# Kernel tuning notes

Hardware: AMD Instinct MI355X
Metric: run time of the kernel (lower is better)

The kernel has to match this reference:

```python
import jax, jax.numpy as jnp
import numpy as np

B, L, D = 4, 1024, 1024
H, DK, DV = 16, 64, 64
TEMP = float(np.power(DK, 0.5))
LN_EPS = 1e-5


def setup_inputs() -> dict:
    key = jax.random.key(0)
    ks = jax.random.split(key, 11)
    s_qk = np.sqrt(2.0 / (D + DK))
    s_v = np.sqrt(2.0 / (D + DV))
    inp = {
        'q_in': jax.random.normal(ks[0], (B, L, D), jnp.float32),
        'k_in': jax.random.normal(ks[1], (B, L, D), jnp.float32),
        'v_in': jax.random.normal(ks[2], (B, L, D), jnp.float32),
        'Wq':  jax.random.normal(ks[3], (D, H * DK), jnp.float32) * s_qk,
        'Wq2': jax.random.normal(ks[4], (D, H * DK), jnp.float32) * s_qk,
        'Wk':  jax.random.normal(ks[5], (D, H * DK), jnp.float32) * s_qk,
        'Wv':  jax.random.normal(ks[6], (D, H * DV), jnp.float32) * s_v,
        'Wo':  jax.random.normal(ks[7], (H * DV, D), jnp.float32) * np.sqrt(2.0 / (H * DV + D)),
        'ln_g': jnp.ones((D,), jnp.float32),
        'ln_b': jnp.zeros((D,), jnp.float32),
        'Er':  jax.random.normal(ks[8], (H, L, DK), jnp.float32),
        # causal mask: True above the diagonal (positions to be masked with -inf)
        'mask': jnp.triu(jnp.ones((L, L), jnp.bool_), k=1)[None].repeat(B, axis=0),
    }
    return inp


def _skew(rel):
    # rel: [H, B, Lq, Lr] with Lr == Lq. Music-Transformer skew:
    # pad one zero column on the left, reshape, drop first row.
    h, b, lq, lr = rel.shape
    rel = jnp.pad(rel, ((0, 0), (0, 0), (0, 0), (1, 0)))        # [H,B,Lq,Lr+1]
    rel = rel.reshape(h, b, lr + 1, lq)                          # [H,B,Lr+1,Lq]
    return rel[:, :, 1:, :].reshape(h, b, lq, lr)                # [H,B,Lq,Lr]


def reference(q_in, k_in, v_in, Wq, Wq2, Wk, Wv, Wo, ln_g, ln_b, Er, mask):
    residual = q_in
    # projections -> [H, B, L, d]
    def proj(x, W, d):
        return x.reshape(B * L, D).dot(W).reshape(B, L, H, d).transpose(2, 0, 1, 3)
    q = proj(q_in, Wq, DK)
    q2 = proj(q_in, Wq2, DK)
    k = proj(k_in, Wk, DK)
    v = proj(v_in, Wv, DV)

    attn = jnp.einsum('hbqd,hbkd->hbqk', q, k) / TEMP            # [H,B,Lq,Lk]
    rel = _skew(jnp.einsum('hbqd,hrd->hbqr', q2, Er)) / TEMP     # [H,B,Lq,Lk]

    m = mask[None]                                               # [1,B,Lq,Lk]
    neg = jnp.float32(-jnp.inf)
    attn = jnp.where(m, neg, attn)
    rel = jnp.where(m, neg, rel)
    p = jax.nn.softmax(attn + rel, axis=-1)                      # [H,B,Lq,Lk]

    out = jnp.einsum('hbqk,hbkd->hbqd', p, v)                    # [H,B,Lq,DV]
    out = out.transpose(1, 2, 0, 3).reshape(B, L, H * DV)
    out = out.dot(Wo)                                            # dropout is identity (eval)

    x = out + residual
    mu = x.mean(-1, keepdims=True)
    var = x.var(-1, keepdims=True)
    y = (x - mu) * jax.lax.rsqrt(var + LN_EPS) * ln_g + ln_b
    return y, p
```

## Files before the change

kernel.cpp:

```cpp
#include <hip/hip_runtime.h>

typedef __bf16 bf16;
typedef __bf16 v8bf __attribute__((ext_vector_type(8)));
typedef float v4f __attribute__((ext_vector_type(4)));
typedef unsigned int v4u __attribute__((ext_vector_type(4)));

#define B_ 4
#define L_ 1024
#define D_ 1024
#define NEG (-3.0e38f)
#define MFMA16(a, b, c) __builtin_amdgcn_mfma_f32_16x16x32_bf16(a, b, c, 0, 0, 0)

#define SWZ(base, r, cb) ((char*)(base) + ((r) * 128) + ((cb) ^ (((r) & 7) << 4)))

typedef const __attribute__((address_space(1))) void* gas_t;
typedef __attribute__((address_space(3))) void* las_t;
__device__ __forceinline__ void gl_lds16(const bf16* g, bf16* l)
{
    __builtin_amdgcn_global_load_lds((gas_t)g, (las_t)l, 16, 0, 0);
}

__global__ __launch_bounds__(256) void wconv_kernel(
    const float* __restrict__ w0, const float* __restrict__ w1,
    const float* __restrict__ w2, const float* __restrict__ w3,
    const float* __restrict__ w4, const float* __restrict__ er,
    const float* __restrict__ qin, const float* __restrict__ kin,
    const float* __restrict__ vin,
    bf16* __restrict__ wt, bf16* __restrict__ erb,
    bf16* __restrict__ qbf, bf16* __restrict__ kbf, bf16* __restrict__ vbf)
{
    int z = blockIdx.z;
    int tx = threadIdx.x, ty = threadIdx.y;
    if (z < 5) {
        const float* src = z == 0 ? w0 : z == 1 ? w1 : z == 2 ? w2 : z == 3 ? w3 : w4;
        bf16* dst = wt + (size_t)z * 1024 * 1024;
        __shared__ float t[32][33];
        int bx = blockIdx.x * 32, by = blockIdx.y * 32;
#pragma unroll
        for (int i = 0; i < 4; i++)
            t[ty + i * 8][tx] = src[(size_t)(by + ty + i * 8) * 1024 + bx + tx];
        __syncthreads();
#pragma unroll
        for (int i = 0; i < 4; i++)
            dst[(size_t)(bx + ty + i * 8) * 1024 + by + tx] = (bf16)t[tx][ty + i * 8];
    } else if (z == 5) {
        int base = (blockIdx.y * 32 + blockIdx.x) * 256 + ty * 32 + tx;
#pragma unroll
        for (int i = 0; i < 4; i++) {
            int idx = base + i * 262144;
            erb[idx] = (bf16)er[idx];
        }
    } else {
        const float* src = z == 6 ? qin : z == 7 ? kin : vin;
        bf16* dst = z == 6 ? qbf : z == 7 ? kbf : vbf;
        int id = (blockIdx.y * 32 + blockIdx.x) * 256 + ty * 32 + tx;
#pragma unroll
        for (int i = 0; i < 4; i++) {
            int j = id * 4 + i * 1048576;
            float4 v = *(const float4*)(src + j);
            union { bf16 h[4]; uint2 u; } t;
            t.h[0] = (bf16)v.x; t.h[1] = (bf16)v.y;
            t.h[2] = (bf16)v.z; t.h[3] = (bf16)v.w;
            *(uint2*)(dst + j) = t.u;
        }
    }
}

__device__ __forceinline__ void gemm128_core(
    const bf16* __restrict__ Ab, const bf16* __restrict__ Bt,
    float* __restrict__ Cf, bf16* __restrict__ Cb, bf16* __restrict__ Cb2,
    int K, int mode, int tn, int tm,
    bf16* __restrict__ As , bf16* __restrict__ Bs )
{
    int tid = threadIdx.x, lane = tid & 63, w = tid >> 6;
    int wm = (w & 1) * 64, wn = (w >> 1) * 64;
    int m15 = lane & 15, rq = lane >> 4, kq = rq * 8;

    v4f acc[4][4];
#pragma unroll
    for (int m = 0; m < 4; ++m)
#pragma unroll
        for (int n = 0; n < 4; ++n)
#pragma unroll
            for (int i = 0; i < 4; ++i) acc[m][n][i] = 0.f;

    int sr = lane >> 2, scb = (lane & 3) * 8;
    const bf16* ga = Ab + (size_t)(tm + w * 32 + sr) * K + scb;
    const bf16* gb = Bt + (size_t)(tn + w * 32 + sr) * K + scb;
    bf16* la = As + w * 32 * 32;
    bf16* lb = Bs + w * 32 * 32;
    const size_t rowskip = (size_t)16 * K;

    for (int k0 = 0; k0 < K; k0 += 32) {
        gl_lds16(ga + k0, la);
        gl_lds16(ga + k0 + rowskip, la + 512);
        gl_lds16(gb + k0, lb);
        gl_lds16(gb + k0 + rowskip, lb + 512);
        __syncthreads();

        v8bf a[4], bfr[4];
#pragma unroll
        for (int m = 0; m < 4; ++m)
            a[m] = *(const v8bf*)&As[(wm + m * 16 + m15) * 32 + kq];
#pragma unroll
        for (int n = 0; n < 4; ++n)
            bfr[n] = *(const v8bf*)&Bs[(wn + n * 16 + m15) * 32 + kq];
#pragma unroll
        for (int m = 0; m < 4; ++m)
#pragma unroll
            for (int n = 0; n < 4; ++n)
                acc[m][n] = MFMA16(a[m], bfr[n], acc[m][n]);
        __syncthreads();
    }

#pragma unroll
    for (int m = 0; m < 4; ++m)
#pragma unroll
        for (int n = 0; n < 4; ++n) {
            int col = tn + wn + n * 16 + m15;
            if (mode == 2) {
                union { bf16 h[4]; uint2 u; } pk;
#pragma unroll
                for (int i = 0; i < 4; ++i) pk.h[i] = (bf16)acc[m][n][i];
                int row0 = tm + wm + m * 16 + rq * 4;
                int bb2 = row0 >> 10, l = row0 & 1023, hh = col >> 6, dv = col & 63;
                *(uint2*)&Cb[(((size_t)(bb2 * 16 + hh) * 64 + dv) << 10) + l] = pk.u;
            } else {
#pragma unroll
                for (int i = 0; i < 4; ++i) {
                    int row = tm + wm + m * 16 + rq * 4 + i;
                    float v = acc[m][n][i];
                    if (mode == 1) Cf[(size_t)row * 1024 + col] = v;
                    else {
                        bf16* dst = col < 1024 ? Cb : Cb2;
                        dst[(size_t)row * 1024 + (col & 1023)] = (bf16)v;
                    }
                }
            }
        }
}

__global__ __launch_bounds__(256) void gemm_proj(
    const bf16* __restrict__ qbf, const bf16* __restrict__ kbf,
    const bf16* __restrict__ vbf, const bf16* __restrict__ wT,
    bf16* __restrict__ qb, bf16* __restrict__ q2b,
    bf16* __restrict__ kb, bf16* __restrict__ vtb)
{
    __shared__ __align__(16) bf16 As[128 * 32];
    __shared__ __align__(16) bf16 Bs[128 * 32];
    int bx = blockIdx.x, tm = blockIdx.y * 128;
    const size_t MB = 1024 * 1024;
    if (bx < 16)
        gemm128_core(qbf, wT, nullptr, qb, q2b, 1024, 0, bx * 128, tm, As, Bs);
    else if (bx < 24)
        gemm128_core(kbf, wT + 2 * MB, nullptr, kb, nullptr, 1024, 0,
                     (bx - 16) * 128, tm, As, Bs);
    else
        gemm128_core(vbf, wT + 3 * MB, nullptr, vtb, nullptr, 1024, 2,
                     (bx - 24) * 128, tm, As, Bs);
}

__global__ __launch_bounds__(256) void gemm_out(
    const bf16* __restrict__ ab, const bf16* __restrict__ woT,
    float* __restrict__ y0)
{
    __shared__ __align__(16) bf16 As[128 * 32];
    __shared__ __align__(16) bf16 Bs[128 * 32];
    gemm128_core(ab, woT, y0, nullptr, nullptr, 1024, 1,
                 blockIdx.x * 128, blockIdx.y * 128, As, Bs);
}

__global__ __launch_bounds__(256, 2) void attn_mfma(
    const bf16* __restrict__ qb, const bf16* __restrict__ q2b,
    const bf16* __restrict__ kb, const bf16* __restrict__ vt,
    const bf16* __restrict__ erb, float* __restrict__ p_out,
    bf16* __restrict__ ab)
{
    int lin = blockIdx.x;
    int bh  = (lin & 7) | ((lin >> 6) << 3);
    int pp  = (lin >> 3) & 7;
    int h = bh >> 2, b = bh & 3;
    int tid = threadIdx.x, lane = tid & 63, w = tid >> 6;
    int m15 = lane & 15, rq = lane >> 4, kq = rq * 8;
    int li0 = w * 16 + rq * 4;

    __shared__ __align__(16) char KsB[2][8192];
    __shared__ __align__(16) char VtsB[2][8192];
    __shared__ __align__(16) char ErsB[3][8192];
    __shared__ __align__(16) float RELs[64][68];
    char* RELsB = (char*)RELs;

    size_t pb = (size_t)(h * 4 + b) << 20;
    size_t kbase = ((size_t)(b << 10) * 16 + h) * 64;
    size_t vbase = ((size_t)(b * 16 + h) << 16);
    const bf16* erh = erb + ((size_t)h << 16);

    int c0 = tid, c1 = tid + 256;
    int r0s = c0 >> 3, col0 = (c0 & 7) * 8, cb0 = (c0 & 7) * 16;
    int r1s = c1 >> 3, col1 = (c1 & 7) * 8, cb1 = (c1 & 7) * 16;

#define LOADK(d0, d1, kt) { int kk = (kt) << 6; \
    d0 = *(const uint4*)&kb[kbase + ((size_t)(kk + r0s) << 10) + col0]; \
    d1 = *(const uint4*)&kb[kbase + ((size_t)(kk + r1s) << 10) + col1]; }
#define LOADE(d0, d1, t) { const bf16* e = erh + ((size_t)(t) << 12); \
    d0 = *(const uint4*)&e[(r0s << 6) + col0]; \
    d1 = *(const uint4*)&e[(r1s << 6) + col1]; }
#define LOADV(d0, d1, kt) { int kk = (kt) << 6; \
    d0 = *(const uint4*)&vt[vbase + ((size_t)r0s << 10) + kk + col0]; \
    d1 = *(const uint4*)&vt[vbase + ((size_t)r1s << 10) + kk + col1]; }
#define STORE2(buf, v0, v1) { *(uint4*)SWZ(buf, r0s, cb0) = v0; \
                              *(uint4*)SWZ(buf, r1s, cb1) = v1; }

    for (int qs = 0; qs < 2; ++qs) {
        int qt = qs ? pp : 15 - pp;
        int q0 = qt << 6, nkt = qt + 1, t0 = 15 - qt;

        {
            int zr = tid >> 2, zc = (tid & 3) * 16;
            v4f zz = {0.f, 0.f, 0.f, 0.f};
            for (int kt = qt + 1; kt < 16; ++kt) {
                float* basep = p_out + pb + ((size_t)(q0 + zr) << 10) + kt * 64 + zc;
#pragma unroll
                for (int i = 0; i < 4; ++i)
                    __builtin_nontemporal_store(zz, (v4f*)(basep + i * 4));
            }
        }

        {
            uint4 a0 = *(const uint4*)&qb[((size_t)((b << 10) + q0 + r0s) * 16 + h) * 64 + col0];
            uint4 a1 = *(const uint4*)&qb[((size_t)((b << 10) + q0 + r1s) * 16 + h) * 64 + col1];
            uint4 b0 = *(const uint4*)&q2b[((size_t)((b << 10) + q0 + r0s) * 16 + h) * 64 + col0];
            uint4 b1 = *(const uint4*)&q2b[((size_t)((b << 10) + q0 + r1s) * 16 + h) * 64 + col1];
            STORE2(RELsB, a0, a1);
            STORE2(RELsB + 8192, b0, b1);
        }
        __syncthreads();
        v8bf alo  = *(const v8bf*)SWZ(RELsB,        w * 16 + m15, kq * 2);
        v8bf ahi  = *(const v8bf*)SWZ(RELsB,        w * 16 + m15, kq * 2 + 64);
        v8bf a2lo = *(const v8bf*)SWZ(RELsB + 8192, w * 16 + m15, kq * 2);
        v8bf a2hi = *(const v8bf*)SWZ(RELsB + 8192, w * 16 + m15, kq * 2 + 64);

        float m_run[4], l_run[4], linv[4];
#pragma unroll
        for (int i = 0; i < 4; ++i) { m_run[i] = NEG; l_run[i] = 0.f; }
        v4f oacc[4];
#pragma unroll
        for (int t = 0; t < 4; ++t)
#pragma unroll
            for (int i = 0; i < 4; ++i) oacc[t][i] = 0.f;

        for (int pass = 0; pass < 2; ++pass) {
            if (pass) {
#pragma unroll
                for (int i = 0; i < 4; ++i) linv[i] = 1.f / l_run[i];
            }
            {
                uint4 ka, kb2, e0a, e0b, e1a, e1b, va, vb2;
                LOADK(ka, kb2, 0);
                LOADE(e0a, e0b, t0);
                bool hb = (t0 + 1) <= 15;
                if (hb) LOADE(e1a, e1b, t0 + 1);
                if (pass) LOADV(va, vb2, 0);
                STORE2(KsB[0], ka, kb2);
                STORE2(ErsB[t0 % 3], e0a, e0b);
                if (hb) STORE2(ErsB[(t0 + 1) % 3], e1a, e1b);
                if (pass) STORE2(VtsB[0], va, vb2);
            }
            __syncthreads();

            uint4 nk0, nk1, ne0, ne1, nv0, nv1;
            for (int kt = 0; kt < nkt; ++kt) {
                int k0 = kt << 6;
                int tA = t0 + kt;
                bool hasB = tA < 15;
                bool hasNext = (kt + 1) < nkt;
                bool hasNE = hasNext && (tA + 2) <= 15;
                if (hasNext) {
                    LOADK(nk0, nk1, kt + 1);
                    if (hasNE) LOADE(ne0, ne1, tA + 2);
                    if (pass) LOADV(nv0, nv1, kt + 1);
                }
                char* Kb = KsB[kt & 1];
                char* EA = ErsB[tA % 3];
                char* EB = ErsB[(tA + 1) % 3];
                char* Vb = VtsB[kt & 1];

                __builtin_amdgcn_s_setprio(1);
#pragma unroll
                for (int ct = 0; ct < 4; ++ct) {
                    v4f a4 = {0.f, 0.f, 0.f, 0.f};
                    v8bf blo = *(const v8bf*)SWZ(EA, ct * 16 + m15, kq * 2);
                    v8bf bhi = *(const v8bf*)SWZ(EA, ct * 16 + m15, kq * 2 + 64);
                    a4 = MFMA16(a2lo, blo, a4);
                    a4 = MFMA16(a2hi, bhi, a4);
                    int c = ct * 16 + m15;
#pragma unroll
                    for (int i = 0; i < 4; ++i) {
                        int kl = c + li0 + i - 63;
                        if (kl >= 0) RELs[li0 + i][kl] = a4[i];
                    }
                }
                if (hasB) {
#pragma unroll
                    for (int ct = 0; ct < 4; ++ct) {
                        v4f a4 = {0.f, 0.f, 0.f, 0.f};
                        v8bf blo = *(const v8bf*)SWZ(EB, ct * 16 + m15, kq * 2);
                        v8bf bhi = *(const v8bf*)SWZ(EB, ct * 16 + m15, kq * 2 + 64);
                        a4 = MFMA16(a2lo, blo, a4);
                        a4 = MFMA16(a2hi, bhi, a4);
                        int c = ct * 16 + m15;
#pragma unroll
                        for (int i = 0; i < 4; ++i) {
                            int kl = c + li0 + i + 1;
                            if (kl < 64) RELs[li0 + i][kl] = a4[i];
                        }
                    }
                }
                v4f qk[4];
#pragma unroll
                for (int ct = 0; ct < 4; ++ct) {
                    v4f a4 = {0.f, 0.f, 0.f, 0.f};
                    v8bf blo = *(const v8bf*)SWZ(Kb, ct * 16 + m15, kq * 2);
                    v8bf bhi = *(const v8bf*)SWZ(Kb, ct * 16 + m15, kq * 2 + 64);
                    a4 = MFMA16(alo, blo, a4);
                    qk[ct] = MFMA16(ahi, bhi, a4);
                }
                __builtin_amdgcn_s_setprio(0);

                float sc[4][4];
#pragma unroll
                for (int ct = 0; ct < 4; ++ct)
#pragma unroll
                    for (int i = 0; i < 4; ++i) {
                        int li = li0 + i;
                        int j = ct * 16 + m15;
                        float v = (qk[ct][i] + RELs[li][j]) * 0.125f;
                        if (!hasB) v = (j > li) ? NEG : v;
                        sc[ct][i] = v;
                    }
                if (!pass) {
#pragma unroll
                    for (int i = 0; i < 4; ++i) {
                        float tmax = fmaxf(fmaxf(sc[0][i], sc[1][i]), fmaxf(sc[2][i], sc[3][i]));
#pragma unroll
                        for (int off = 1; off < 16; off <<= 1)
                            tmax = fmaxf(tmax, __shfl_xor(tmax, off));
                        float mn = fmaxf(m_run[i], tmax);
                        float es = __expf(sc[0][i] - mn) + __expf(sc[1][i] - mn)
                                 + __expf(sc[2][i] - mn) + __expf(sc[3][i] - mn);
#pragma unroll
                        for (int off = 1; off < 16; off <<= 1)
                            es += __shfl_xor(es, off);
                        l_run[i] = l_run[i] * __expf(m_run[i] - mn) + es;
                        m_run[i] = mn;
                    }
                } else {
#pragma unroll
                    for (int ct = 0; ct < 4; ++ct)
#pragma unroll
                        for (int i = 0; i < 4; ++i) {
                            int li = li0 + i;
                            int j = ct * 16 + m15;
                            RELs[li][j] = __expf(sc[ct][i] - m_run[i]) * linv[i];
                        }
                    asm volatile("" ::: "memory");
#pragma unroll
                    for (int i2 = 0; i2 < 2; ++i2)
#pragma unroll
                        for (int jh = 0; jh < 2; ++jh) {
                            int rr = w * 16 + (lane >> 3) + 8 * i2;
                            v4u val = *(const v4u*)(RELsB + rr * 272 + (lane & 7) * 16 + 128 * jh);
                            __builtin_nontemporal_store(val,
                                (v4u*)(p_out + pb + ((size_t)(q0 + rr) << 10) + k0 + (lane & 7) * 4 + 32 * jh));
                        }
                    const float* pr = &RELs[w * 16 + m15][0];
                    v4f f0 = *(const v4f*)(pr + kq);
                    v4f f1 = *(const v4f*)(pr + kq + 4);
                    v4f f2 = *(const v4f*)(pr + kq + 32);
                    v4f f3 = *(const v4f*)(pr + kq + 36);
                    v8bf plo, phi;
#pragma unroll
                    for (int j = 0; j < 4; ++j) {
                        plo[j] = (bf16)f0[j]; plo[j + 4] = (bf16)f1[j];
                        phi[j] = (bf16)f2[j]; phi[j + 4] = (bf16)f3[j];
                    }
                    __builtin_amdgcn_s_setprio(1);
#pragma unroll
                    for (int ct = 0; ct < 4; ++ct) {
                        v8bf blo = *(const v8bf*)SWZ(Vb, ct * 16 + m15, kq * 2);
                        v8bf bhi = *(const v8bf*)SWZ(Vb, ct * 16 + m15, kq * 2 + 64);
                        oacc[ct] = MFMA16(plo, blo, oacc[ct]);
                        oacc[ct] = MFMA16(phi, bhi, oacc[ct]);
                    }
                    __builtin_amdgcn_s_setprio(0);
                }
                if (hasNext) {
                    STORE2(KsB[(kt + 1) & 1], nk0, nk1);
                    if (hasNE) STORE2(ErsB[(tA + 2) % 3], ne0, ne1);
                    if (pass) STORE2(VtsB[(kt + 1) & 1], nv0, nv1);
                }
                __syncthreads();
            }
        }

#pragma unroll
        for (int ct = 0; ct < 4; ++ct)
#pragma unroll
            for (int i = 0; i < 4; ++i)
                ab[((size_t)((b << 10) + q0 + li0 + i) * 16 + h) * 64 + ct * 16 + m15] =
                    (bf16)oacc[ct][i];
    }
#undef LOADK
#undef LOADE
#undef LOADV
#undef STORE2
}

__global__ __launch_bounds__(256) void ln_kernel(
    const float* __restrict__ y0, const float* __restrict__ res,
    const float* __restrict__ g, const float* __restrict__ bb,
    float* __restrict__ y)
{
    int row = blockIdx.x, tid = threadIdx.x, lane = tid & 63, w = tid >> 6;
    __shared__ float rs[4], rq2[4];
    const float* xr = y0 + (size_t)row * D_;
    const float* rr = res + (size_t)row * D_;
    float x[4], sum = 0.f, sq = 0.f;
#pragma unroll
    for (int i = 0; i < 4; i++) {
        int c = tid + i * 256;
        x[i] = xr[c] + rr[c];
        sum += x[i]; sq += x[i] * x[i];
    }
#pragma unroll
    for (int off = 32; off; off >>= 1) { sum += __shfl_xor(sum, off); sq += __shfl_xor(sq, off); }
    if (lane == 0) { rs[w] = sum; rq2[w] = sq; }
    __syncthreads();
    sum = rs[0] + rs[1] + rs[2] + rs[3];
    sq  = rq2[0] + rq2[1] + rq2[2] + rq2[3];
    float mean = sum * (1.f / D_);
    float var  = sq * (1.f / D_) - mean * mean;
    float inv  = rsqrtf(var + 1e-5f);
#pragma unroll
    for (int i = 0; i < 4; i++) {
        int c = tid + i * 256;
        y[(size_t)row * D_ + c] = (x[i] - mean) * inv * g[c] + bb[c];
    }
}

extern "C" void kernel_launch(void* const* d_in, const int* in_sizes, int n_in,
                              void* d_out, int out_size, void* d_ws, size_t ws_size,
                              hipStream_t stream)
{
    const float* q_in = (const float*)d_in[0];
    const float* k_in = (const float*)d_in[1];
    const float* v_in = (const float*)d_in[2];
    const float* Wq   = (const float*)d_in[3];
    const float* Wq2  = (const float*)d_in[4];
    const float* Wk   = (const float*)d_in[5];
    const float* Wv   = (const float*)d_in[6];
    const float* Wo   = (const float*)d_in[7];
    const float* ln_g = (const float*)d_in[8];
    const float* ln_b = (const float*)d_in[9];
    const float* Er   = (const float*)d_in[10];

    float* y_out = (float*)d_out;
    float* p_out = y_out + (size_t)B_ * L_ * D_;

    char* ws = (char*)d_ws;
    const size_t MB = 1024 * 1024;
    bf16*  wT  = (bf16*)(ws);
    bf16*  erb = (bf16*)(ws + 10 * MB);
    bf16*  qb  = (bf16*)(ws + 12 * MB);
    bf16*  q2b = (bf16*)(ws + 20 * MB);
    bf16*  kb  = (bf16*)(ws + 28 * MB);
    bf16*  vtb = (bf16*)(ws + 36 * MB);
    bf16*  ab  = (bf16*)(ws + 44 * MB);
    float* y0  = (float*)(ws + 52 * MB);

    bf16* qbf = (bf16*)((char*)p_out + 160 * MB);
    bf16* kbf = (bf16*)((char*)p_out + 168 * MB);
    bf16* vbf = (bf16*)((char*)p_out + 176 * MB);

    wconv_kernel<<<dim3(32, 32, 9), dim3(32, 8), 0, stream>>>(
        Wq, Wq2, Wk, Wv, Wo, Er, q_in, k_in, v_in, wT, erb, qbf, kbf, vbf);

    gemm_proj<<<dim3(32, 32), 256, 0, stream>>>(qbf, kbf, vbf, wT,
                                                qb, q2b, kb, vtb);

    attn_mfma<<<dim3(512), dim3(256), 0, stream>>>(qb, q2b, kb, vtb, erb, p_out, ab);

    gemm_out<<<dim3(8, 32), 256, 0, stream>>>(ab, wT + 4 * MB, y0);
    ln_kernel<<<4096, 256, 0, stream>>>(y0, q_in, ln_g, ln_b, y_out);
}
```

Measured before the change: 606.7 us.

## Split attention into one block per q-tile, load Er from global, retile output GEMM

The attention kernel now launches one block per (head, batch, q-tile), 1024 blocks, instead of pairing a long and a short q-tile per block. It raises the occupancy hint to 3 blocks per CU and drops the Er LDS triple buffer, so Er fragments are read straight from global memory into MFMA operands. The output projection gets its own 64x128 tiled GEMM, double-buffered via global_load_lds, with twice as many blocks. The aim is more parallelism and occupancy and less LDS. The cost is uncoalesced, uncached-in-LDS Er reads and a heavier tail from the largest q-tiles, which no longer share a block with short ones.

```diff
diff --git a/kernel.cpp b/kernel.cpp
--- a/kernel.cpp
+++ b/kernel.cpp
@@ -161,32 +161,87 @@
 }
 
 __global__ __launch_bounds__(256) void gemm_out(
-    const bf16* __restrict__ ab, const bf16* __restrict__ woT,
-    float* __restrict__ y0)
-{
-    __shared__ __align__(16) bf16 As[128 * 32];
-    __shared__ __align__(16) bf16 Bs[128 * 32];
-    gemm128_core(ab, woT, y0, nullptr, nullptr, 1024, 1,
-                 blockIdx.x * 128, blockIdx.y * 128, As, Bs);
-}
-
-__global__ __launch_bounds__(256, 2) void attn_mfma(
+    const bf16* __restrict__ Ab, const bf16* __restrict__ Bt,
+    float* __restrict__ Cf)
+{
+    const int K = 1024;
+    __shared__ __align__(16) bf16 As[2][64 * 32];
+    __shared__ __align__(16) bf16 Bs[2][128 * 32];
+    int tid = threadIdx.x, lane = tid & 63, w = tid >> 6;
+    int tn = blockIdx.x * 128, tm = blockIdx.y * 64;
+    int wn = w * 32;
+    int m15 = lane & 15, rq = lane >> 4, kq = rq * 8;
+
+    v4f acc[4][2];
+#pragma unroll
+    for (int m = 0; m < 4; ++m)
+#pragma unroll
+        for (int n = 0; n < 2; ++n)
+#pragma unroll
+            for (int i = 0; i < 4; ++i) acc[m][n][i] = 0.f;
+
+    int sr = lane >> 2, sc8 = (lane & 3) * 8;
+    const bf16* ga  = Ab + (size_t)(tm + w * 16 + sr) * K + sc8;
+    const bf16* gb0 = Bt + (size_t)(tn + w * 32 + sr) * K + sc8;
+    const bf16* gb1 = gb0 + (size_t)16 * K;
+
+#define GSTAGE(buf, k0s) { \
+    gl_lds16(ga  + (k0s), As[buf] + w * 16 * 32); \
+    gl_lds16(gb0 + (k0s), Bs[buf] + w * 32 * 32); \
+    gl_lds16(gb1 + (k0s), Bs[buf] + (w * 32 + 16) * 32); }
+
+    int cur = 0;
+    GSTAGE(0, 0);
+    __syncthreads();
+    for (int k0 = 0; k0 < K; k0 += 32) {
+        if (k0 + 32 < K) GSTAGE(cur ^ 1, k0 + 32);
+        v8bf a[4], bb[2];
+#pragma unroll
+        for (int m = 0; m < 4; ++m)
+            a[m] = *(const v8bf*)&As[cur][(m * 16 + m15) * 32 + kq];
+#pragma unroll
+        for (int n = 0; n < 2; ++n)
+            bb[n] = *(const v8bf*)&Bs[cur][(wn + n * 16 + m15) * 32 + kq];
+#pragma unroll
+        for (int m = 0; m < 4; ++m)
+#pragma unroll
+            for (int n = 0; n < 2; ++n)
+                acc[m][n] = MFMA16(a[m], bb[n], acc[m][n]);
+        __syncthreads();
+        cur ^= 1;
+    }
+#undef GSTAGE
+
+#pragma unroll
+    for (int m = 0; m < 4; ++m)
+#pragma unroll
+        for (int n = 0; n < 2; ++n) {
+            int col = tn + wn + n * 16 + m15;
+#pragma unroll
+            for (int i = 0; i < 4; ++i) {
+                int row = tm + m * 16 + rq * 4 + i;
+                Cf[(size_t)row * 1024 + col] = acc[m][n][i];
+            }
+        }
+}
+
+__global__ __launch_bounds__(256, 3) void attn_mfma(
     const bf16* __restrict__ qb, const bf16* __restrict__ q2b,
     const bf16* __restrict__ kb, const bf16* __restrict__ vt,
     const bf16* __restrict__ erb, float* __restrict__ p_out,
     bf16* __restrict__ ab)
 {
     int lin = blockIdx.x;
-    int bh  = (lin & 7) | ((lin >> 6) << 3);
-    int pp  = (lin >> 3) & 7;
+    int bh  = lin & 63;
+    int qt  = 15 - (lin >> 6);
     int h = bh >> 2, b = bh & 3;
+    int q0 = qt << 6, nkt = qt + 1, t0 = 15 - qt;
     int tid = threadIdx.x, lane = tid & 63, w = tid >> 6;
     int m15 = lane & 15, rq = lane >> 4, kq = rq * 8;
     int li0 = w * 16 + rq * 4;
 
     __shared__ __align__(16) char KsB[2][8192];
     __shared__ __align__(16) char VtsB[2][8192];
-    __shared__ __align__(16) char ErsB[3][8192];
     __shared__ __align__(16) float RELs[64][68];
     char* RELsB = (char*)RELs;
 
@@ -202,216 +257,197 @@
 #define LOADK(d0, d1, kt) { int kk = (kt) << 6; \
     d0 = *(const uint4*)&kb[kbase + ((size_t)(kk + r0s) << 10) + col0]; \
     d1 = *(const uint4*)&kb[kbase + ((size_t)(kk + r1s) << 10) + col1]; }
-#define LOADE(d0, d1, t) { const bf16* e = erh + ((size_t)(t) << 12); \
-    d0 = *(const uint4*)&e[(r0s << 6) + col0]; \
-    d1 = *(const uint4*)&e[(r1s << 6) + col1]; }
 #define LOADV(d0, d1, kt) { int kk = (kt) << 6; \
     d0 = *(const uint4*)&vt[vbase + ((size_t)r0s << 10) + kk + col0]; \
     d1 = *(const uint4*)&vt[vbase + ((size_t)r1s << 10) + kk + col1]; }
 #define STORE2(buf, v0, v1) { *(uint4*)SWZ(buf, r0s, cb0) = v0; \
                               *(uint4*)SWZ(buf, r1s, cb1) = v1; }
 
-    for (int qs = 0; qs < 2; ++qs) {
-        int qt = qs ? pp : 15 - pp;
-        int q0 = qt << 6, nkt = qt + 1, t0 = 15 - qt;
-
+    {
+        int zr = tid >> 2, zc = (tid & 3) * 16;
+        v4f zz = {0.f, 0.f, 0.f, 0.f};
+        for (int kt = qt + 1; kt < 16; ++kt) {
+            float* basep = p_out + pb + ((size_t)(q0 + zr) << 10) + kt * 64 + zc;
+#pragma unroll
+            for (int i = 0; i < 4; ++i)
+                __builtin_nontemporal_store(zz, (v4f*)(basep + i * 4));
+        }
+    }
+
+    {
+        uint4 a0 = *(const uint4*)&qb[((size_t)((b << 10) + q0 + r0s) * 16 + h) * 64 + col0];
+        uint4 a1 = *(const uint4*)&qb[((size_t)((b << 10) + q0 + r1s) * 16 + h) * 64 + col1];
+        uint4 b0 = *(const uint4*)&q2b[((size_t)((b << 10) + q0 + r0s) * 16 + h) * 64 + col0];
+        uint4 b1 = *(const uint4*)&q2b[((size_t)((b << 10) + q0 + r1s) * 16 + h) * 64 + col1];
+        STORE2(RELsB, a0, a1);
+        STORE2(RELsB + 8192, b0, b1);
+    }
+    __syncthreads();
+    v8bf alo  = *(const v8bf*)SWZ(RELsB,        w * 16 + m15, kq * 2);
+    v8bf ahi  = *(const v8bf*)SWZ(RELsB,        w * 16 + m15, kq * 2 + 64);
+    v8bf a2lo = *(const v8bf*)SWZ(RELsB + 8192, w * 16 + m15, kq * 2);
+    v8bf a2hi = *(const v8bf*)SWZ(RELsB + 8192, w * 16 + m15, kq * 2 + 64);
+
+    float m_run[4], l_run[4], linv[4];
+#pragma unroll
+    for (int i = 0; i < 4; ++i) { m_run[i] = NEG; l_run[i] = 0.f; }
+    v4f oacc[4];
+#pragma unroll
+    for (int t = 0; t < 4; ++t)
+#pragma unroll
+        for (int i = 0; i < 4; ++i) oacc[t][i] = 0.f;
+
+    for (int pass = 0; pass < 2; ++pass) {
+        if (pass) {
+#pragma unroll
+            for (int i = 0; i < 4; ++i) linv[i] = 1.f / l_run[i];
+        }
         {
-            int zr = tid >> 2, zc = (tid & 3) * 16;
-            v4f zz = {0.f, 0.f, 0.f, 0.f};
-            for (int kt = qt + 1; kt < 16; ++kt) {
-                float* basep = p_out + pb + ((size_t)(q0 + zr) << 10) + kt * 64 + zc;
-#pragma unroll
-                for (int i = 0; i < 4; ++i)
-                    __builtin_nontemporal_store(zz, (v4f*)(basep + i * 4));
-            }
-        }
-
-        {
-            uint4 a0 = *(const uint4*)&qb[((size_t)((b << 10) + q0 + r0s) * 16 + h) * 64 + col0];
-            uint4 a1 = *(const uint4*)&qb[((size_t)((b << 10) + q0 + r1s) * 16 + h) * 64 + col1];
-            uint4 b0 = *(const uint4*)&q2b[((size_t)((b << 10) + q0 + r0s) * 16 + h) * 64 + col0];
-            uint4 b1 = *(const uint4*)&q2b[((size_t)((b << 10) + q0 + r1s) * 16 + h) * 64 + col1];
-            STORE2(RELsB, a0, a1);
-            STORE2(RELsB + 8192, b0, b1);
+            uint4 ka, kb2, va, vb2;
+            LOADK(ka, kb2, 0);
+            if (pass) LOADV(va, vb2, 0);
+            STORE2(KsB[0], ka, kb2);
+            if (pass) STORE2(VtsB[0], va, vb2);
         }
         __syncthreads();
-        v8bf alo  = *(const v8bf*)SWZ(RELsB,        w * 16 + m15, kq * 2);
-        v8bf ahi  = *(const v8bf*)SWZ(RELsB,        w * 16 + m15, kq * 2 + 64);
-        v8bf a2lo = *(const v8bf*)SWZ(RELsB + 8192, w * 16 + m15, kq * 2);
-        v8bf a2hi = *(const v8bf*)SWZ(RELsB + 8192, w * 16 + m15, kq * 2 + 64);
-
-        float m_run[4], l_run[4], linv[4];
-#pragma unroll
-        for (int i = 0; i < 4; ++i) { m_run[i] = NEG; l_run[i] = 0.f; }
-        v4f oacc[4];
-#pragma unroll
-        for (int t = 0; t < 4; ++t)
-#pragma unroll
-            for (int i = 0; i < 4; ++i) oacc[t][i] = 0.f;
-
-        for (int pass = 0; pass < 2; ++pass) {
-            if (pass) {
-#pragma unroll
-                for (int i = 0; i < 4; ++i) linv[i] = 1.f / l_run[i];
-            }
-            {
-                uint4 ka, kb2, e0a, e0b, e1a, e1b, va, vb2;
-                LOADK(ka, kb2, 0);
-                LOADE(e0a, e0b, t0);
-                bool hb = (t0 + 1) <= 15;
-                if (hb) LOADE(e1a, e1b, t0 + 1);
-                if (pass) LOADV(va, vb2, 0);
-                STORE2(KsB[0], ka, kb2);
-                STORE2(ErsB[t0 % 3], e0a, e0b);
-                if (hb) STORE2(ErsB[(t0 + 1) % 3], e1a, e1b);
-                if (pass) STORE2(VtsB[0], va, vb2);
-            }
-            __syncthreads();
-
-            uint4 nk0, nk1, ne0, ne1, nv0, nv1;
-            for (int kt = 0; kt < nkt; ++kt) {
-                int k0 = kt << 6;
-                int tA = t0 + kt;
-                bool hasB = tA < 15;
-                bool hasNext = (kt + 1) < nkt;
-                bool hasNE = hasNext && (tA + 2) <= 15;
-                if (hasNext) {
-                    LOADK(nk0, nk1, kt + 1);
-                    if (hasNE) LOADE(ne0, ne1, tA + 2);
-                    if (pass) LOADV(nv0, nv1, kt + 1);
-                }
-                char* Kb = KsB[kt & 1];
-                char* EA = ErsB[tA % 3];
-                char* EB = ErsB[(tA + 1) % 3];
-                char* Vb = VtsB[kt & 1];
-
-                __builtin_amdgcn_s_setprio(1);
+
+        uint4 nk0, nk1, nv0, nv1;
+        for (int kt = 0; kt < nkt; ++kt) {
+            int k0 = kt << 6;
+            int tA = t0 + kt;
+            bool hasB = tA < 15;
+            bool hasNext = (kt + 1) < nkt;
+            if (hasNext) {
+                LOADK(nk0, nk1, kt + 1);
+                if (pass) LOADV(nv0, nv1, kt + 1);
+            }
+            char* Kb = KsB[kt & 1];
+            char* Vb = VtsB[kt & 1];
+            const bf16* eA = erh + ((size_t)tA << 12);
+
+            __builtin_amdgcn_s_setprio(1);
+#pragma unroll
+            for (int ct = 0; ct < 4; ++ct) {
+                const bf16* er_ = eA + (ct * 16 + m15) * 64;
+                v4f a4 = {0.f, 0.f, 0.f, 0.f};
+                a4 = MFMA16(a2lo, *(const v8bf*)(er_ + kq), a4);
+                a4 = MFMA16(a2hi, *(const v8bf*)(er_ + kq + 32), a4);
+                int c = ct * 16 + m15;
+#pragma unroll
+                for (int i = 0; i < 4; ++i) {
+                    int kl = c + li0 + i - 63;
+                    if (kl >= 0) RELs[li0 + i][kl] = a4[i];
+                }
+            }
+            if (hasB) {
+                const bf16* eB = eA + 4096;
 #pragma unroll
                 for (int ct = 0; ct < 4; ++ct) {
+                    const bf16* er_ = eB + (ct * 16 + m15) * 64;
                     v4f a4 = {0.f, 0.f, 0.f, 0.f};
-                    v8bf blo = *(const v8bf*)SWZ(EA, ct * 16 + m15, kq * 2);
-                    v8bf bhi = *(const v8bf*)SWZ(EA, ct * 16 + m15, kq * 2 + 64);
-                    a4 = MFMA16(a2lo, blo, a4);
-                    a4 = MFMA16(a2hi, bhi, a4);
+                    a4 = MFMA16(a2lo, *(const v8bf*)(er_ + kq), a4);
+                    a4 = MFMA16(a2hi, *(const v8bf*)(er_ + kq + 32), a4);
                     int c = ct * 16 + m15;
 #pragma unroll
                     for (int i = 0; i < 4; ++i) {
-                        int kl = c + li0 + i - 63;
-                        if (kl >= 0) RELs[li0 + i][kl] = a4[i];
+                        int kl = c + li0 + i + 1;
+                        if (kl < 64) RELs[li0 + i][kl] = a4[i];
                     }
                 }
-                if (hasB) {
-#pragma unroll
-                    for (int ct = 0; ct < 4; ++ct) {
-                        v4f a4 = {0.f, 0.f, 0.f, 0.f};
-                        v8bf blo = *(const v8bf*)SWZ(EB, ct * 16 + m15, kq * 2);
-                        v8bf bhi = *(const v8bf*)SWZ(EB, ct * 16 + m15, kq * 2 + 64);
-                        a4 = MFMA16(a2lo, blo, a4);
-                        a4 = MFMA16(a2hi, bhi, a4);
-                        int c = ct * 16 + m15;
-#pragma unroll
-                        for (int i = 0; i < 4; ++i) {
-                            int kl = c + li0 + i + 1;
-                            if (kl < 64) RELs[li0 + i][kl] = a4[i];
-                        }
-                    }
-                }
-                v4f qk[4];
-#pragma unroll
-                for (int ct = 0; ct < 4; ++ct) {
-                    v4f a4 = {0.f, 0.f, 0.f, 0.f};
-                    v8bf blo = *(const v8bf*)SWZ(Kb, ct * 16 + m15, kq * 2);
-                    v8bf bhi = *(const v8bf*)SWZ(Kb, ct * 16 + m15, kq * 2 + 64);
-                    a4 = MFMA16(alo, blo, a4);
-                    qk[ct] = MFMA16(ahi, bhi, a4);
-                }
-                __builtin_amdgcn_s_setprio(0);
-
-                float sc[4][4];
+            }
+            v4f qk[4];
+#pragma unroll
+            for (int ct = 0; ct < 4; ++ct) {
+                v4f a4 = {0.f, 0.f, 0.f, 0.f};
+                v8bf blo = *(const v8bf*)SWZ(Kb, ct * 16 + m15, kq * 2);
+                v8bf bhi = *(const v8bf*)SWZ(Kb, ct * 16 + m15, kq * 2 + 64);
+                a4 = MFMA16(alo, blo, a4);
+                qk[ct] = MFMA16(ahi, bhi, a4);
+            }
+            __builtin_amdgcn_s_setprio(0);
+
+            float sc[4][4];
+#pragma unroll
+            for (int ct = 0; ct < 4; ++ct)
+#pragma unroll
+                for (int i = 0; i < 4; ++i) {
+                    int li = li0 + i;
+                    int j = ct * 16 + m15;
+                    float v = (qk[ct][i] + RELs[li][j]) * 0.125f;
+                    if (!hasB) v = (j > li) ? NEG : v;
+                    sc[ct][i] = v;
+                }
+            if (!pass) {
+#pragma unroll
+                for (int i = 0; i < 4; ++i) {
+                    float tmax = fmaxf(fmaxf(sc[0][i], sc[1][i]), fmaxf(sc[2][i], sc[3][i]));
+#pragma unroll
+                    for (int off = 1; off < 16; off <<= 1)
+                        tmax = fmaxf(tmax, __shfl_xor(tmax, off));
+                    float mn = fmaxf(m_run[i], tmax);
+                    float es = __expf(sc[0][i] - mn) + __expf(sc[1][i] - mn)
+                             + __expf(sc[2][i] - mn) + __expf(sc[3][i] - mn);
+#pragma unroll
+                    for (int off = 1; off < 16; off <<= 1)
+                        es += __shfl_xor(es, off);
+                    l_run[i] = l_run[i] * __expf(m_run[i] - mn) + es;
+                    m_run[i] = mn;
+                }
+            } else {
 #pragma unroll
                 for (int ct = 0; ct < 4; ++ct)
 #pragma unroll
                     for (int i = 0; i < 4; ++i) {
                         int li = li0 + i;
                         int j = ct * 16 + m15;
-                        float v = (qk[ct][i] + RELs[li][j]) * 0.125f;
-                        if (!hasB) v = (j > li) ? NEG : v;
-                        sc[ct][i] = v;
+                        RELs[li][j] = __expf(sc[ct][i] - m_run[i]) * linv[i];
                     }
-                if (!pass) {
-#pragma unroll
-                    for (int i = 0; i < 4; ++i) {
-                        float tmax = fmaxf(fmaxf(sc[0][i], sc[1][i]), fmaxf(sc[2][i], sc[3][i]));
-#pragma unroll
-                        for (int off = 1; off < 16; off <<= 1)
-                            tmax = fmaxf(tmax, __shfl_xor(tmax, off));
-                        float mn = fmaxf(m_run[i], tmax);
-                        float es = __expf(sc[0][i] - mn) + __expf(sc[1][i] - mn)
-                                 + __expf(sc[2][i] - mn) + __expf(sc[3][i] - mn);
-#pragma unroll
-                        for (int off = 1; off < 16; off <<= 1)
-                            es += __shfl_xor(es, off);
-                        l_run[i] = l_run[i] * __expf(m_run[i] - mn) + es;
-                        m_run[i] = mn;
+                asm volatile("" ::: "memory");
+#pragma unroll
+                for (int i2 = 0; i2 < 2; ++i2)
+#pragma unroll
+                    for (int jh = 0; jh < 2; ++jh) {
+                        int rr = w * 16 + (lane >> 3) + 8 * i2;
+                        v4u val = *(const v4u*)(RELsB + rr * 272 + (lane & 7) * 16 + 128 * jh);
+                        __builtin_nontemporal_store(val,
+                            (v4u*)(p_out + pb + ((size_t)(q0 + rr) << 10) + k0 + (lane & 7) * 4 + 32 * jh));
                     }
-                } else {
-#pragma unroll
-                    for (int ct = 0; ct < 4; ++ct)
-#pragma unroll
-                        for (int i = 0; i < 4; ++i) {
-                            int li = li0 + i;
-                            int j = ct * 16 + m15;
-                            RELs[li][j] = __expf(sc[ct][i] - m_run[i]) * linv[i];
-                        }
-                    asm volatile("" ::: "memory");
-#pragma unroll
-                    for (int i2 = 0; i2 < 2; ++i2)
-#pragma unroll
-                        for (int jh = 0; jh < 2; ++jh) {
-                            int rr = w * 16 + (lane >> 3) + 8 * i2;
-                            v4u val = *(const v4u*)(RELsB + rr * 272 + (lane & 7) * 16 + 128 * jh);
-                            __builtin_nontemporal_store(val,
-                                (v4u*)(p_out + pb + ((size_t)(q0 + rr) << 10) + k0 + (lane & 7) * 4 + 32 * jh));
-                        }
-                    const float* pr = &RELs[w * 16 + m15][0];
-                    v4f f0 = *(const v4f*)(pr + kq);
-                    v4f f1 = *(const v4f*)(pr + kq + 4);
-                    v4f f2 = *(const v4f*)(pr + kq + 32);
-                    v4f f3 = *(const v4f*)(pr + kq + 36);
-                    v8bf plo, phi;
-#pragma unroll
-                    for (int j = 0; j < 4; ++j) {
-                        plo[j] = (bf16)f0[j]; plo[j + 4] = (bf16)f1[j];
-                        phi[j] = (bf16)f2[j]; phi[j + 4] = (bf16)f3[j];
-                    }
-                    __builtin_amdgcn_s_setprio(1);
-#pragma unroll
-                    for (int ct = 0; ct < 4; ++ct) {
-                        v8bf blo = *(const v8bf*)SWZ(Vb, ct * 16 + m15, kq * 2);
-                        v8bf bhi = *(const v8bf*)SWZ(Vb, ct * 16 + m15, kq * 2 + 64);
-                        oacc[ct] = MFMA16(plo, blo, oacc[ct]);
-                        oacc[ct] = MFMA16(phi, bhi, oacc[ct]);
-                    }
-                    __builtin_amdgcn_s_setprio(0);
-                }
-                if (hasNext) {
-                    STORE2(KsB[(kt + 1) & 1], nk0, nk1);
-                    if (hasNE) STORE2(ErsB[(tA + 2) % 3], ne0, ne1);
-                    if (pass) STORE2(VtsB[(kt + 1) & 1], nv0, nv1);
-                }
-                __syncthreads();
-            }
-        }
-
-#pragma unroll
-        for (int ct = 0; ct < 4; ++ct)
-#pragma unroll
-            for (int i = 0; i < 4; ++i)
-                ab[((size_t)((b << 10) + q0 + li0 + i) * 16 + h) * 64 + ct * 16 + m15] =
-                    (bf16)oacc[ct][i];
-    }
+                const float* pr = &RELs[w * 16 + m15][0];
+                v4f f0 = *(const v4f*)(pr + kq);
+                v4f f1 = *(const v4f*)(pr + kq + 4);
+                v4f f2 = *(const v4f*)(pr + kq + 32);
+                v4f f3 = *(const v4f*)(pr + kq + 36);
+                v8bf plo, phi;
+#pragma unroll
+                for (int j = 0; j < 4; ++j) {
+                    plo[j] = (bf16)f0[j]; plo[j + 4] = (bf16)f1[j];
+                    phi[j] = (bf16)f2[j]; phi[j + 4] = (bf16)f3[j];
+                }
+                __builtin_amdgcn_s_setprio(1);
+#pragma unroll
+                for (int ct = 0; ct < 4; ++ct) {
+                    v8bf blo = *(const v8bf*)SWZ(Vb, ct * 16 + m15, kq * 2);
+                    v8bf bhi = *(const v8bf*)SWZ(Vb, ct * 16 + m15, kq * 2 + 64);
+                    oacc[ct] = MFMA16(plo, blo, oacc[ct]);
+                    oacc[ct] = MFMA16(phi, bhi, oacc[ct]);
+                }
+                __builtin_amdgcn_s_setprio(0);
+            }
+            if (hasNext) {
+                STORE2(KsB[(kt + 1) & 1], nk0, nk1);
+                if (pass) STORE2(VtsB[(kt + 1) & 1], nv0, nv1);
+            }
+            __syncthreads();
+        }
+    }
+
+#pragma unroll
+    for (int ct = 0; ct < 4; ++ct)
+#pragma unroll
+        for (int i = 0; i < 4; ++i)
+            ab[((size_t)((b << 10) + q0 + li0 + i) * 16 + h) * 64 + ct * 16 + m15] =
+                (bf16)oacc[ct][i];
 #undef LOADK
-#undef LOADE
 #undef LOADV
 #undef STORE2
 }
@@ -488,8 +524,8 @@
     gemm_proj<<<dim3(32, 32), 256, 0, stream>>>(qbf, kbf, vbf, wT,
                                                 qb, q2b, kb, vtb);
 
-    attn_mfma<<<dim3(512), dim3(256), 0, stream>>>(qb, q2b, kb, vtb, erb, p_out, ab);
-
-    gemm_out<<<dim3(8, 32), 256, 0, stream>>>(ab, wT + 4 * MB, y0);
+    attn_mfma<<<dim3(1024), dim3(256), 0, stream>>>(qb, q2b, kb, vtb, erb, p_out, ab);
+
+    gemm_out<<<dim3(8, 64), 256, 0, stream>>>(ab, wT + 4 * MB, y0);
     ln_kernel<<<4096, 256, 0, stream>>>(y0, q_in, ln_g, ln_b, y_out);
 }
```

Measured after the change: 642.6 us. 5.9% more time.
